# Kernel tuning notes

Measured on AMD Instinct MI355X. Metric: run time of the kernel, lower is better.

The kernel has to match this reference:

```python
import jax, jax.numpy as jnp
import numpy as np
import math

FS, N_FFT, NUM_BANDS, NUM_BINS = 16000, 512, 31, 257
H = 96  # dim_hidden

def band_partition():
    f_min, f_max = FS / N_FFT, FS / 2.0
    z_min = 69.0 + 12.0 * math.log2(f_min / 440.0)
    z_max = 69.0 + 12.0 * math.log2(f_max / 440.0)
    z = np.linspace(z_min, z_max, NUM_BANDS + 2)
    f_points = 440.0 * 2.0 ** ((z - 69.0) / 12.0)
    bins = np.round(f_points * N_FFT / FS).astype(np.int64)
    bins[0] = 0
    bands = []
    for i in range(NUM_BANDS):
        s = max(0, int(bins[i]))
        e = min(NUM_BINS, int(bins[i + 2]) + 1)
        if e <= s:
            e = s + 1
        bands.append((s, e))
    return bands

BANDS = band_partition()

def hann(L):
    # torch.hann_window default (periodic=True)
    return 0.5 - 0.5 * jnp.cos(2.0 * jnp.pi * jnp.arange(L, dtype=jnp.float32) / L)

def chan_ln(x, eps=1e-5):
    # AdaNorm2d assumed = LayerNorm over channel dim, no affine
    m = jnp.mean(x, axis=1, keepdims=True)
    v = jnp.var(x, axis=1, keepdims=True)
    return (x - m) * jax.lax.rsqrt(v + eps)

def prelu(x, a):
    return jnp.where(x >= 0, x, a * x)

def setup_inputs() -> dict:
    key = jax.random.key(0)
    ks = jax.random.split(key, 20)
    B, T = 4, 1000
    return {
        'mix_repr': jax.random.normal(ks[0], (B, H, NUM_BINS, T), jnp.float32),
        'spin': jax.random.normal(ks[1], (B, 64, NUM_BINS, T), jnp.float32),
        'doa': jax.random.normal(ks[2], (B, 36), jnp.float32),
        'enc_w': jax.random.normal(ks[3], (NUM_BANDS, H, 64), jnp.float32) * 0.05,
        'enc_b': jax.random.normal(ks[4], (NUM_BANDS, H), jnp.float32) * 0.05,
        'enc_a': 0.25 * jnp.ones((NUM_BANDS,), jnp.float32),
        'dqg_w': jax.random.normal(ks[5], (NUM_BANDS, 2 * H, 36), jnp.float32) * 0.05,
        'dqg_b': jax.random.normal(ks[6], (NUM_BANDS, 2 * H), jnp.float32) * 0.05,
        'dec_w': jax.random.normal(ks[7], (NUM_BANDS, H, H), jnp.float32) * 0.05,
        'dec_b': jax.random.normal(ks[8], (NUM_BANDS, H), jnp.float32) * 0.05,
        'dec_a': 0.25 * jnp.ones((NUM_BANDS,), jnp.float32),
        'qw': jax.random.normal(ks[9], (H, H), jnp.float32) * 0.05,
        'qb': jax.random.normal(ks[10], (H,), jnp.float32) * 0.05,
        'kw': jax.random.normal(ks[11], (H, H), jnp.float32) * 0.05,
        'kb': jax.random.normal(ks[12], (H,), jnp.float32) * 0.05,
        'vw': jax.random.normal(ks[13], (H, H), jnp.float32) * 0.05,
        'vb': jax.random.normal(ks[14], (H,), jnp.float32) * 0.05,
        'ow': jax.random.normal(ks[15], (H, H), jnp.float32) * 0.05,
        'ob': jax.random.normal(ks[16], (H,), jnp.float32) * 0.05,
    }

def reference(mix_repr, spin, doa, enc_w, enc_b, enc_a, dqg_w, dqg_b,
              dec_w, dec_b, dec_a, qw, qb, kw, kb, vw, vb, ow, ob):
    B, D, F, T = mix_repr.shape
    merged = jnp.zeros((B, H, F, T), mix_repr.dtype)
    wsum = jnp.zeros((F,), mix_repr.dtype)
    for k, (s, e) in enumerate(BANDS):  # fixed set of 31 static ragged bands
        L = e - s
        win = hann(L)
        sub = spin[:, :, s:e, :]                                   # [B,64,L,T]
        feat = jnp.einsum('oc,bcft->boft', enc_w[k], sub) + enc_b[k][None, :, None, None]
        feat = prelu(chan_ln(feat), enc_a[k])
        qp = doa @ dqg_w[k].T + dqg_b[k]                           # [B,2H]
        gamma, beta = qp[:, :H], qp[:, H:]
        tgt = (1.0 + gamma)[:, :, None, None] * feat + beta[:, :, None, None]
        dec = jnp.einsum('oc,bcft->boft', dec_w[k], tgt) + dec_b[k][None, :, None, None]
        dec = prelu(chan_ln(dec), dec_a[k])
        merged = merged.at[:, :, s:e, :].add(dec * win[None, None, :, None])
        wsum = wsum.at[s:e].add(win)
    merged = merged / jnp.clip(wsum, 1e-8)[None, None, :, None]
    # MixtureQueryFusion: 1x1 conv cross-attention gate
    Q = jnp.einsum('oc,bcft->boft', qw, mix_repr) + qb[None, :, None, None]
    K = jnp.einsum('oc,bcft->boft', kw, merged) + kb[None, :, None, None]
    V = jnp.einsum('oc,bcft->boft', vw, merged) + vb[None, :, None, None]
    attn = jax.nn.sigmoid(jnp.sum(Q * K, axis=1, keepdims=True) / jnp.sqrt(jnp.float32(H)))
    attended = V * attn
    out = mix_repr + jnp.einsum('oc,bcft->boft', ow, attended) + ob[None, :, None, None]
    return out
```

## Files before the change

kernel.cpp:

```cpp
#include <hip/hip_runtime.h>
#include <math.h>

#define NBANDS 31
#define FT 257000

typedef __attribute__((ext_vector_type(8))) short bh8;
typedef __attribute__((ext_vector_type(4))) float f4;

__constant__ int d_bs[NBANDS] = {0,1,1,2,2,2,3,3,4,5,6,7,8,10,11,13,16,19,23,27,32,38,45,54,64,76,91,108,128,152,181};
__constant__ int d_be[NBANDS] = {2,3,3,3,4,4,5,6,7,8,9,11,12,14,17,20,24,28,33,39,46,55,65,77,92,109,129,153,182,216,257};

__device__ __forceinline__ unsigned short b16u(float v) {
  __bf16 h = (__bf16)v;
  return __builtin_bit_cast(unsigned short, h);
}
__device__ __forceinline__ unsigned pk2(float a, float b) {
  return (unsigned)b16u(a) | ((unsigned)b16u(b) << 16);
}
__device__ __forceinline__ float hann1(int i, int L) {
  return 0.5f - 0.5f * cosf(6.283185307179586f * (float)i / (float)L);
}

__global__ __launch_bounds__(256) void prep_w(
    const float* __restrict__ enc_w, const float* __restrict__ dec_w,
    const float* __restrict__ qw, const float* __restrict__ kw,
    const float* __restrict__ vw, const float* __restrict__ ow,
    unsigned short* __restrict__ w16) {
  const int stride = gridDim.x * blockDim.x;
  for (int i = blockIdx.x * blockDim.x + threadIdx.x; i < 513024; i += stride) {
    float v;
    if (i < 190464) {
      const int k = i / 6144, r = i - k * 6144;
      const int tile = r >> 9, li = r & 511;
      const int lane = li >> 3, j = li & 7;
      const int g = lane >> 4, n = lane & 15;
      const int mt = tile >> 1, kt = tile & 1;
      v = enc_w[k * 6144 + (mt * 16 + n) * 64 + kt * 32 + g * 8 + j];
    } else if (i < 476160) {
      const int i2 = i - 190464;
      const int k = i2 / 9216, r = i2 - k * 9216;
      const int tile = r >> 9, li = r & 511;
      const int lane = li >> 3, j = li & 7;
      const int g = lane >> 4, n = lane & 15;
      const int mt = tile / 3, kt = tile - mt * 3;
      v = dec_w[k * 9216 + (mt * 16 + n) * 96 + kt * 32 + g * 8 + j];
    } else {
      const int i2 = i - 476160;
      const int a = i2 / 9216, r = i2 - a * 9216;
      const int tile = r >> 9, li = r & 511;
      const int lane = li >> 3, j = li & 7;
      const int g = lane >> 4, n = lane & 15;
      const int mt = tile / 3, kt = tile - mt * 3;
      const float* src = (a == 0) ? qw : (a == 1) ? kw : (a == 2) ? vw : ow;
      v = src[(mt * 16 + n) * 96 + kt * 32 + g * 8 + j];
    }
    w16[i] = b16u(v);
  }
}

__global__ __launch_bounds__(192) void qp_kernel(const float* __restrict__ doa,
                                                 const float* __restrict__ dqg_w,
                                                 const float* __restrict__ dqg_b,
                                                 float* __restrict__ gbuf) {
  const int k = blockIdx.x, b = blockIdx.y;
  const int tid = threadIdx.x;
  __shared__ float sdoa[36];
  if (tid < 36) sdoa[tid] = doa[b * 36 + tid];
  __syncthreads();
  const float* wr = dqg_w + (k * 192 + tid) * 36;
  float acc = dqg_b[k * 192 + tid];
  #pragma unroll
  for (int i = 0; i < 36; ++i) acc = fmaf(wr[i], sdoa[i], acc);
  if (tid < 96) acc += 1.0f;
  gbuf[(k * 4 + b) * 192 + tid] = acc;
}

__global__ __launch_bounds__(320) void tab_kernel(float* __restrict__ ftab) {
  const int f = blockIdx.x * blockDim.x + threadIdx.x;
  if (f >= 257) return;
  int k0 = 0; while (d_be[k0] <= f) ++k0;
  int k1 = k0; while (k1 < NBANDS && d_bs[k1] <= f) ++k1;
  float wsum = 0.f, wn[5];
  for (int k = k0; k < k1; ++k) {
    const float wv = hann1(f - d_bs[k], d_be[k] - d_bs[k]);
    wn[k - k0] = wv; wsum += wv;
  }
  float* o = ftab + f * 8;
  o[0] = (float)k0; o[1] = (float)(k1 - k0); o[2] = 1.0f / fmaxf(wsum, 1e-8f);
  #pragma unroll
  for (int j = 0; j < 5; ++j) o[3 + j] = (j < k1 - k0) ? wn[j] : 0.f;
}

#define LDSWAIT asm volatile("s_waitcnt lgkmcnt(0)" ::: "memory")

__device__ __forceinline__ void init6(f4* acc, const float* s, int off) {
  #pragma unroll
  for (int mt = 0; mt < 6; ++mt) {
    const float4 bb = *reinterpret_cast<const float4*>(s + mt * 16 + off);
    acc[mt] = (f4){bb.x, bb.y, bb.z, bb.w};
  }
}
__device__ __forceinline__ f4 init1(const float* s, int mt, int off) {
  const float4 bb = *reinterpret_cast<const float4*>(s + mt * 16 + off);
  return (f4){bb.x, bb.y, bb.z, bb.w};
}
__device__ __forceinline__ void ln96(const f4* acc, float& mean, float& rs) {
  float sm = 0.f, sq = 0.f;
  #pragma unroll
  for (int mt = 0; mt < 6; ++mt)
    #pragma unroll
    for (int r = 0; r < 4; ++r) { const float v = acc[mt][r]; sm += v; sq = fmaf(v, v, sq); }
  sm += __shfl_xor(sm, 16); sm += __shfl_xor(sm, 32);
  sq += __shfl_xor(sq, 16); sq += __shfl_xor(sq, 32);
  mean = sm * (1.f / 96.f);
  rs = rsqrtf(sq * (1.f / 96.f) - mean * mean + 1e-5f);
}
__device__ __forceinline__ void load6s(bh8* dst, const unsigned short* p, int step9) {
  #pragma unroll
  for (int mt = 0; mt < 6; ++mt)
    dst[mt] = *reinterpret_cast<const bh8*>(p + ((mt * step9) << 9));
}

__global__ __launch_bounds__(256, 4) void fused_mfma(
    const float* __restrict__ mix, const float* __restrict__ spin,
    const unsigned short* __restrict__ enc16, const float* __restrict__ enc_b, const float* __restrict__ enc_a,
    const unsigned short* __restrict__ dec16, const float* __restrict__ dec_b, const float* __restrict__ dec_a,
    const float* __restrict__ gb, const float* __restrict__ ftab,
    const unsigned short* __restrict__ q16, const float* __restrict__ qb,
    const unsigned short* __restrict__ k16, const float* __restrict__ kb,
    const unsigned short* __restrict__ v16, const float* __restrict__ vb,
    const unsigned short* __restrict__ o16, const float* __restrict__ ob,
    float* __restrict__ out) {
  const int id0 = (int)blockIdx.x;
  const int id  = (id0 & 7) * 2056 + (id0 >> 3);
  const int tt  = id & 15;
  const int fb  = id >> 4;
  const int f   = fb % 257;
  const int b   = fb / 257;
  const int t0  = tt << 6;

  const int tid  = threadIdx.x;
  const int lane = tid & 63;
  const int w    = tid >> 6;
  const int g    = lane >> 4;
  const int n    = lane & 15;
  const int col  = (w << 4) + n;
  const int t    = t0 + col;
  const bool tv  = t < 1000;
  const int tcl  = tv ? t : 999;
  const int sw   = (n & 7) << 3;
  const int lb   = lane << 3;

  __shared__ __align__(16) unsigned short XT[64 * 128];
  __shared__ __align__(16) float stage[5 * 512 + 384];
  unsigned short* xw = XT + col * 128;

  const float* ft = ftab + f * 8;
  const int k0 = (int)ft[0];
  const int nb = (int)ft[1];
  const float winv = ft[2];

  {
    const int tot = (nb << 9) + 384;
    for (int i = tid; i < tot; i += 256) {
      const int kk = i >> 9, r = i & 511;
      float v = 0.f;
      if (kk < nb) {
        const int k = k0 + kk;
        if      (r < 96)  v = enc_b[k * 96 + r];
        else if (r < 192) v = dec_b[k * 96 + (r - 96)];
        else if (r < 384) v = gb[(k * 4 + b) * 192 + (r - 192)];
        else if (r == 384) v = enc_a[k];
        else if (r == 385) v = dec_a[k];
        else if (r == 386) v = ft[3 + kk];
      } else {
        const int r2 = i - (nb << 9);
        v = (r2 < 96) ? qb[r2] : (r2 < 192) ? kb[r2 - 96] : (r2 < 288) ? vb[r2 - 192] : ob[r2 - 288];
      }
      stage[i] = v;
    }
  }

  const float* spL = spin + b * 64 * FT + f * 1000 + tcl;
  const float* mxL = mix  + b * 96 * FT + f * 1000 + tcl;

  bh8 spb[2];
  {
    float spf[16];
    #pragma unroll
    for (int j = 0; j < 8; ++j) spf[j]     = __builtin_nontemporal_load(spL + (g * 8 + j) * FT);
    #pragma unroll
    for (int j = 0; j < 8; ++j) spf[8 + j] = __builtin_nontemporal_load(spL + (32 + g * 8 + j) * FT);
    #pragma unroll
    for (int kt = 0; kt < 2; ++kt)
      #pragma unroll
      for (int j = 0; j < 8; ++j) spb[kt][j] = (short)b16u(spf[kt * 8 + j]);
  }

  bh8 pre[6];
  load6s(pre, enc16 + k0 * 6144 + lb, 2);

  __syncthreads();

  f4 macc[6];
  #pragma unroll
  for (int mt = 0; mt < 6; ++mt) macc[mt] = (f4){0.f, 0.f, 0.f, 0.f};

  const int oo = g * 4;

  for (int kk = 0; kk < nb; ++kk) {
    const int k = k0 + kk;
    const unsigned short* ew  = enc16 + k * 6144 + lb;
    const unsigned short* dwp = dec16 + k * 9216 + lb;
    const float* stg = stage + (kk << 9);

    f4 acc[6];
    init6(acc, stg, oo);
    #pragma unroll
    for (int mt = 0; mt < 6; ++mt)
      acc[mt] = __builtin_amdgcn_mfma_f32_16x16x32_bf16(pre[mt], spb[0], acc[mt], 0, 0, 0);
    #pragma unroll
    for (int mt = 0; mt < 6; ++mt) {
      const bh8 af = *reinterpret_cast<const bh8*>(ew + ((mt * 2 + 1) << 9));
      acc[mt] = __builtin_amdgcn_mfma_f32_16x16x32_bf16(af, spb[1], acc[mt], 0, 0, 0);
    }

    load6s(pre, dwp, 3);

    float mean, rs;
    ln96(acc, mean, rs);
    const float ea = stg[384];
    #pragma unroll
    for (int mt = 0; mt < 6; ++mt) {
      const float4 ga = *reinterpret_cast<const float4*>(stg + 192 + mt * 16 + oo);
      const float4 be = *reinterpret_cast<const float4*>(stg + 288 + mt * 16 + oo);
      float x0 = (acc[mt][0] - mean) * rs; x0 = (x0 >= 0.f) ? x0 : ea * x0;
      float x1 = (acc[mt][1] - mean) * rs; x1 = (x1 >= 0.f) ? x1 : ea * x1;
      float x2 = (acc[mt][2] - mean) * rs; x2 = (x2 >= 0.f) ? x2 : ea * x2;
      float x3 = (acc[mt][3] - mean) * rs; x3 = (x3 >= 0.f) ? x3 : ea * x3;
      uint2 u;
      u.x = pk2(fmaf(ga.x, x0, be.x), fmaf(ga.y, x1, be.y));
      u.y = pk2(fmaf(ga.z, x2, be.z), fmaf(ga.w, x3, be.w));
      *reinterpret_cast<uint2*>(xw + ((mt * 16 + g * 4) ^ sw)) = u;
    }
    LDSWAIT;

    f4 dacc[6];
    init6(dacc, stg + 96, oo);
    {
      const bh8 bf0 = *reinterpret_cast<const bh8*>(xw + ((0 * 32 + g * 8) ^ sw));
      #pragma unroll
      for (int mt = 0; mt < 6; ++mt)
        dacc[mt] = __builtin_amdgcn_mfma_f32_16x16x32_bf16(pre[mt], bf0, dacc[mt], 0, 0, 0);
    }

    {
      const bool more = (kk + 1 < nb);
      load6s(pre, more ? (enc16 + (k + 1) * 6144 + lb) : (q16 + lb), more ? 2 : 3);
    }

    #pragma unroll
    for (int kt = 1; kt < 3; ++kt) {
      const bh8 bf = *reinterpret_cast<const bh8*>(xw + ((kt * 32 + g * 8) ^ sw));
      #pragma unroll
      for (int mt = 0; mt < 6; ++mt) {
        const bh8 af = *reinterpret_cast<const bh8*>(dwp + ((mt * 3 + kt) << 9));
        dacc[mt] = __builtin_amdgcn_mfma_f32_16x16x32_bf16(af, bf, dacc[mt], 0, 0, 0);
      }
    }
    float mean2, rs2;
    ln96(dacc, mean2, rs2);
    const float da = stg[385];
    const float win = stg[386];
    #pragma unroll
    for (int mt = 0; mt < 6; ++mt)
      #pragma unroll
      for (int r = 0; r < 4; ++r) {
        float x = (dacc[mt][r] - mean2) * rs2;
        x = (x >= 0.f) ? x : da * x;
        macc[mt][r] = fmaf(win, x, macc[mt][r]);
      }
  }

  bh8 mxb[3];
  {
    float mxf[24];
    #pragma unroll
    for (int kt = 0; kt < 3; ++kt)
      #pragma unroll
      for (int j = 0; j < 8; ++j) mxf[kt * 8 + j] = mxL[(kt * 32 + g * 8 + j) * FT];
    #pragma unroll
    for (int kt = 0; kt < 3; ++kt)
      #pragma unroll
      for (int j = 0; j < 8; ++j) mxb[kt][j] = (short)b16u(mxf[kt * 8 + j]);
  }

  #pragma unroll
  for (int mt = 0; mt < 6; ++mt) {
    uint2 u;
    u.x = pk2(macc[mt][0] * winv, macc[mt][1] * winv);
    u.y = pk2(macc[mt][2] * winv, macc[mt][3] * winv);
    *reinterpret_cast<uint2*>(xw + ((mt * 16 + g * 4) ^ sw)) = u;
  }
  LDSWAIT;
  bh8 gfr[3];
  #pragma unroll
  for (int kt = 0; kt < 3; ++kt) gfr[kt] = *reinterpret_cast<const bh8*>(xw + ((kt * 32 + g * 8) ^ sw));

  const float* stQ = stage + (nb << 9);
  const unsigned short* qp16 = q16 + lb;
  const unsigned short* kp16 = k16 + lb;
  const unsigned short* vp16 = v16 + lb;
  const unsigned short* op16 = o16 + lb;

  float p = 0.f;
  #pragma unroll
  for (int mt = 0; mt < 6; ++mt) {
    f4 qa = init1(stQ, mt, oo);
    qa = __builtin_amdgcn_mfma_f32_16x16x32_bf16(pre[mt], mxb[0], qa, 0, 0, 0);
    #pragma unroll
    for (int kt = 1; kt < 3; ++kt) {
      const bh8 af = *reinterpret_cast<const bh8*>(qp16 + ((mt * 3 + kt) << 9));
      qa = __builtin_amdgcn_mfma_f32_16x16x32_bf16(af, mxb[kt], qa, 0, 0, 0);
    }
    f4 ka = init1(stQ + 96, mt, oo);
    #pragma unroll
    for (int kt = 0; kt < 3; ++kt) {
      const bh8 af = *reinterpret_cast<const bh8*>(kp16 + ((mt * 3 + kt) << 9));
      ka = __builtin_amdgcn_mfma_f32_16x16x32_bf16(af, gfr[kt], ka, 0, 0, 0);
    }
    #pragma unroll
    for (int r = 0; r < 4; ++r) p = fmaf(qa[r], ka[r], p);
  }
  p += __shfl_xor(p, 16); p += __shfl_xor(p, 32);
  const float sig = 1.f / (1.f + __expf(-p * 0.10206207261596575f));

  #pragma unroll
  for (int mt = 0; mt < 6; ++mt) {
    f4 va = init1(stQ + 192, mt, oo);
    #pragma unroll
    for (int kt = 0; kt < 3; ++kt) {
      const bh8 af = *reinterpret_cast<const bh8*>(vp16 + ((mt * 3 + kt) << 9));
      va = __builtin_amdgcn_mfma_f32_16x16x32_bf16(af, gfr[kt], va, 0, 0, 0);
    }
    uint2 u;
    u.x = pk2(va[0] * sig, va[1] * sig);
    u.y = pk2(va[2] * sig, va[3] * sig);
    *reinterpret_cast<uint2*>(xw + ((mt * 16 + g * 4) ^ sw)) = u;
  }
  float mres[6][4];
  #pragma unroll
  for (int mt = 0; mt < 6; ++mt)
    #pragma unroll
    for (int r = 0; r < 4; ++r) mres[mt][r] = mxL[(mt * 16 + g * 4 + r) * FT];
  LDSWAIT;
  bh8 afr[3];
  #pragma unroll
  for (int kt = 0; kt < 3; ++kt) afr[kt] = *reinterpret_cast<const bh8*>(xw + ((kt * 32 + g * 8) ^ sw));

  #pragma unroll
  for (int mt = 0; mt < 6; ++mt) {
    f4 oa = init1(stQ + 288, mt, oo);
    #pragma unroll
    for (int kt = 0; kt < 3; ++kt) {
      const bh8 af = *reinterpret_cast<const bh8*>(op16 + ((mt * 3 + kt) << 9));
      oa = __builtin_amdgcn_mfma_f32_16x16x32_bf16(af, afr[kt], oa, 0, 0, 0);
    }
    if (tv) {
      const int base = (b * 96 + mt * 16 + g * 4) * FT + f * 1000 + t;
      #pragma unroll
      for (int r = 0; r < 4; ++r)
        __builtin_nontemporal_store(mres[mt][r] + oa[r], out + base + r * FT);
    }
  }
}

extern "C" void kernel_launch(void* const* d_in, const int* in_sizes, int n_in,
                              void* d_out, int out_size, void* d_ws, size_t ws_size,
                              hipStream_t stream) {
  (void)in_sizes; (void)n_in; (void)out_size; (void)ws_size;
  const float* mix   = (const float*)d_in[0];
  const float* spin  = (const float*)d_in[1];
  const float* doa   = (const float*)d_in[2];
  const float* enc_w = (const float*)d_in[3];
  const float* enc_b = (const float*)d_in[4];
  const float* enc_a = (const float*)d_in[5];
  const float* dqg_w = (const float*)d_in[6];
  const float* dqg_b = (const float*)d_in[7];
  const float* dec_w = (const float*)d_in[8];
  const float* dec_b = (const float*)d_in[9];
  const float* dec_a = (const float*)d_in[10];
  const float* qw    = (const float*)d_in[11];
  const float* qb    = (const float*)d_in[12];
  const float* kw    = (const float*)d_in[13];
  const float* kb    = (const float*)d_in[14];
  const float* vw    = (const float*)d_in[15];
  const float* vb    = (const float*)d_in[16];
  const float* oww   = (const float*)d_in[17];
  const float* obb   = (const float*)d_in[18];
  float* outp = (float*)d_out;

  unsigned short* w16 = (unsigned short*)d_ws;
  unsigned short* enc16 = w16;
  unsigned short* dec16 = w16 + 190464;
  unsigned short* q16   = w16 + 476160;
  unsigned short* k16   = q16 + 9216;
  unsigned short* v16   = k16 + 9216;
  unsigned short* o16   = v16 + 9216;
  float* gbws = (float*)((char*)d_ws + 1026048);
  float* ftab = (float*)((char*)d_ws + 1121280);

  hipLaunchKernelGGL(prep_w, dim3(512), dim3(256), 0, stream,
                     enc_w, dec_w, qw, kw, vw, oww, w16);
  hipLaunchKernelGGL(qp_kernel, dim3(NBANDS, 4), dim3(192), 0, stream,
                     doa, dqg_w, dqg_b, gbws);
  hipLaunchKernelGGL(tab_kernel, dim3(1), dim3(320), 0, stream, ftab);
  hipLaunchKernelGGL(fused_mfma, dim3(16448), dim3(256), 0, stream,
                     mix, spin, enc16, enc_b, enc_a, dec16, dec_b, dec_a, gbws, ftab,
                     q16, qb, k16, kb, v16, vb, o16, obb, outp);
}
```

Measured before the change: 671.8 us.

## Keep merged accumulator and mix residual in LDS as bf16, drop second mix read

Several changes at once. The band accumulator moves from 24 float registers into a bf16 LDS tile, and the staged biases and gammas are stored as bf16. The mix input, already loaded once for Q, is stashed in LDS and reused as the residual, so the second global read of mix_repr goes away. This cuts global traffic and register pressure, but the residual, the accumulated merge and the biases now carry bf16 rounding error.

```diff
diff --git a/kernel.cpp b/kernel.cpp
--- a/kernel.cpp
+++ b/kernel.cpp
@@ -19,6 +19,15 @@
 }
 __device__ __forceinline__ float hann1(int i, int L) {
   return 0.5f - 0.5f * cosf(6.283185307179586f * (float)i / (float)L);
+}
+__device__ __forceinline__ f4 bf4(const unsigned short* p) {
+  const uint2 u = *reinterpret_cast<const uint2*>(p);
+  f4 r;
+  r[0] = __builtin_bit_cast(float, u.x << 16);
+  r[1] = __builtin_bit_cast(float, u.x & 0xffff0000u);
+  r[2] = __builtin_bit_cast(float, u.y << 16);
+  r[3] = __builtin_bit_cast(float, u.y & 0xffff0000u);
+  return r;
 }
 
 __global__ __launch_bounds__(256) void prep_w(
@@ -93,17 +102,6 @@
 
 #define LDSWAIT asm volatile("s_waitcnt lgkmcnt(0)" ::: "memory")
 
-__device__ __forceinline__ void init6(f4* acc, const float* s, int off) {
-  #pragma unroll
-  for (int mt = 0; mt < 6; ++mt) {
-    const float4 bb = *reinterpret_cast<const float4*>(s + mt * 16 + off);
-    acc[mt] = (f4){bb.x, bb.y, bb.z, bb.w};
-  }
-}
-__device__ __forceinline__ f4 init1(const float* s, int mt, int off) {
-  const float4 bb = *reinterpret_cast<const float4*>(s + mt * 16 + off);
-  return (f4){bb.x, bb.y, bb.z, bb.w};
-}
 __device__ __forceinline__ void ln96(const f4* acc, float& mean, float& rs) {
   float sm = 0.f, sq = 0.f;
   #pragma unroll
@@ -152,8 +150,11 @@
   const int lb   = lane << 3;
 
   __shared__ __align__(16) unsigned short XT[64 * 128];
-  __shared__ __align__(16) float stage[5 * 512 + 384];
+  __shared__ __align__(16) unsigned short MG[64 * 128];
+  __shared__ __align__(16) unsigned short stgb[5 * 512 + 384];
+  __shared__ float sband[5 * 4];
   unsigned short* xw = XT + col * 128;
+  unsigned short* mg = MG + col * 128;
 
   const float* ft = ftab + f * 8;
   const int k0 = (int)ft[0];
@@ -170,14 +171,16 @@
         if      (r < 96)  v = enc_b[k * 96 + r];
         else if (r < 192) v = dec_b[k * 96 + (r - 96)];
         else if (r < 384) v = gb[(k * 4 + b) * 192 + (r - 192)];
-        else if (r == 384) v = enc_a[k];
-        else if (r == 385) v = dec_a[k];
-        else if (r == 386) v = ft[3 + kk];
       } else {
         const int r2 = i - (nb << 9);
         v = (r2 < 96) ? qb[r2] : (r2 < 192) ? kb[r2 - 96] : (r2 < 288) ? vb[r2 - 192] : ob[r2 - 288];
       }
-      stage[i] = v;
+      stgb[i] = b16u(v);
+    }
+    if (tid < nb * 4) {
+      const int kk = tid >> 2, j = tid & 3;
+      sband[tid] = (j == 0) ? enc_a[k0 + kk] : (j == 1) ? dec_a[k0 + kk]
+                 : (j == 2) ? ft[3 + kk] : 0.f;
     }
   }
 
@@ -201,10 +204,6 @@
   load6s(pre, enc16 + k0 * 6144 + lb, 2);
 
   __syncthreads();
-
-  f4 macc[6];
-  #pragma unroll
-  for (int mt = 0; mt < 6; ++mt) macc[mt] = (f4){0.f, 0.f, 0.f, 0.f};
 
   const int oo = g * 4;
 
@@ -212,10 +211,11 @@
     const int k = k0 + kk;
     const unsigned short* ew  = enc16 + k * 6144 + lb;
     const unsigned short* dwp = dec16 + k * 9216 + lb;
-    const float* stg = stage + (kk << 9);
+    const unsigned short* stg = stgb + (kk << 9);
 
     f4 acc[6];
-    init6(acc, stg, oo);
+    #pragma unroll
+    for (int mt = 0; mt < 6; ++mt) acc[mt] = bf4(stg + mt * 16 + oo);
     #pragma unroll
     for (int mt = 0; mt < 6; ++mt)
       acc[mt] = __builtin_amdgcn_mfma_f32_16x16x32_bf16(pre[mt], spb[0], acc[mt], 0, 0, 0);
@@ -229,24 +229,25 @@
 
     float mean, rs;
     ln96(acc, mean, rs);
-    const float ea = stg[384];
+    const float ea = sband[kk * 4];
     #pragma unroll
     for (int mt = 0; mt < 6; ++mt) {
-      const float4 ga = *reinterpret_cast<const float4*>(stg + 192 + mt * 16 + oo);
-      const float4 be = *reinterpret_cast<const float4*>(stg + 288 + mt * 16 + oo);
+      const f4 ga = bf4(stg + 192 + mt * 16 + oo);
+      const f4 be = bf4(stg + 288 + mt * 16 + oo);
       float x0 = (acc[mt][0] - mean) * rs; x0 = (x0 >= 0.f) ? x0 : ea * x0;
       float x1 = (acc[mt][1] - mean) * rs; x1 = (x1 >= 0.f) ? x1 : ea * x1;
       float x2 = (acc[mt][2] - mean) * rs; x2 = (x2 >= 0.f) ? x2 : ea * x2;
       float x3 = (acc[mt][3] - mean) * rs; x3 = (x3 >= 0.f) ? x3 : ea * x3;
       uint2 u;
-      u.x = pk2(fmaf(ga.x, x0, be.x), fmaf(ga.y, x1, be.y));
-      u.y = pk2(fmaf(ga.z, x2, be.z), fmaf(ga.w, x3, be.w));
-      *reinterpret_cast<uint2*>(xw + ((mt * 16 + g * 4) ^ sw)) = u;
+      u.x = pk2(fmaf(ga[0], x0, be[0]), fmaf(ga[1], x1, be[1]));
+      u.y = pk2(fmaf(ga[2], x2, be[2]), fmaf(ga[3], x3, be[3]));
+      *reinterpret_cast<uint2*>(xw + ((mt * 16 + oo) ^ sw)) = u;
     }
     LDSWAIT;
 
     f4 dacc[6];
-    init6(dacc, stg + 96, oo);
+    #pragma unroll
+    for (int mt = 0; mt < 6; ++mt) dacc[mt] = bf4(stg + 96 + mt * 16 + oo);
     {
       const bh8 bf0 = *reinterpret_cast<const bh8*>(xw + ((0 * 32 + g * 8) ^ sw));
       #pragma unroll
@@ -270,16 +271,26 @@
     }
     float mean2, rs2;
     ln96(dacc, mean2, rs2);
-    const float da = stg[385];
-    const float win = stg[386];
-    #pragma unroll
-    for (int mt = 0; mt < 6; ++mt)
-      #pragma unroll
-      for (int r = 0; r < 4; ++r) {
-        float x = (dacc[mt][r] - mean2) * rs2;
-        x = (x >= 0.f) ? x : da * x;
-        macc[mt][r] = fmaf(win, x, macc[mt][r]);
+    const float da  = sband[kk * 4 + 1];
+    const float win = sband[kk * 4 + 2];
+    #pragma unroll
+    for (int mt = 0; mt < 6; ++mt) {
+      float x0 = (dacc[mt][0] - mean2) * rs2; x0 = (x0 >= 0.f) ? x0 : da * x0;
+      float x1 = (dacc[mt][1] - mean2) * rs2; x1 = (x1 >= 0.f) ? x1 : da * x1;
+      float x2 = (dacc[mt][2] - mean2) * rs2; x2 = (x2 >= 0.f) ? x2 : da * x2;
+      float x3 = (dacc[mt][3] - mean2) * rs2; x3 = (x3 >= 0.f) ? x3 : da * x3;
+      unsigned short* mp = mg + ((mt * 16 + oo) ^ sw);
+      uint2 u;
+      if (kk == 0) {
+        u.x = pk2(win * x0, win * x1);
+        u.y = pk2(win * x2, win * x3);
+      } else {
+        const f4 cur = bf4(mp);
+        u.x = pk2(fmaf(win, x0, cur[0]), fmaf(win, x1, cur[1]));
+        u.y = pk2(fmaf(win, x2, cur[2]), fmaf(win, x3, cur[3]));
       }
+      *reinterpret_cast<uint2*>(mp) = u;
+    }
   }
 
   bh8 mxb[3];
@@ -288,7 +299,7 @@
     #pragma unroll
     for (int kt = 0; kt < 3; ++kt)
       #pragma unroll
-      for (int j = 0; j < 8; ++j) mxf[kt * 8 + j] = mxL[(kt * 32 + g * 8 + j) * FT];
+      for (int j = 0; j < 8; ++j) mxf[kt * 8 + j] = __builtin_nontemporal_load(mxL + (kt * 32 + g * 8 + j) * FT);
     #pragma unroll
     for (int kt = 0; kt < 3; ++kt)
       #pragma unroll
@@ -297,17 +308,22 @@
 
   #pragma unroll
   for (int mt = 0; mt < 6; ++mt) {
+    const f4 mv = bf4(mg + ((mt * 16 + oo) ^ sw));
     uint2 u;
-    u.x = pk2(macc[mt][0] * winv, macc[mt][1] * winv);
-    u.y = pk2(macc[mt][2] * winv, macc[mt][3] * winv);
-    *reinterpret_cast<uint2*>(xw + ((mt * 16 + g * 4) ^ sw)) = u;
+    u.x = pk2(mv[0] * winv, mv[1] * winv);
+    u.y = pk2(mv[2] * winv, mv[3] * winv);
+    *reinterpret_cast<uint2*>(xw + ((mt * 16 + oo) ^ sw)) = u;
   }
   LDSWAIT;
   bh8 gfr[3];
   #pragma unroll
   for (int kt = 0; kt < 3; ++kt) gfr[kt] = *reinterpret_cast<const bh8*>(xw + ((kt * 32 + g * 8) ^ sw));
 
-  const float* stQ = stage + (nb << 9);
+  #pragma unroll
+  for (int kt = 0; kt < 3; ++kt)
+    *reinterpret_cast<bh8*>(mg + ((kt * 32 + g * 8) ^ sw)) = mxb[kt];
+
+  const unsigned short* stQ = stgb + (nb << 9);
   const unsigned short* qp16 = q16 + lb;
   const unsigned short* kp16 = k16 + lb;
   const unsigned short* vp16 = v16 + lb;
@@ -316,14 +332,14 @@
   float p = 0.f;
   #pragma unroll
   for (int mt = 0; mt < 6; ++mt) {
-    f4 qa = init1(stQ, mt, oo);
+    f4 qa = bf4(stQ + mt * 16 + oo);
     qa = __builtin_amdgcn_mfma_f32_16x16x32_bf16(pre[mt], mxb[0], qa, 0, 0, 0);
     #pragma unroll
     for (int kt = 1; kt < 3; ++kt) {
       const bh8 af = *reinterpret_cast<const bh8*>(qp16 + ((mt * 3 + kt) << 9));
       qa = __builtin_amdgcn_mfma_f32_16x16x32_bf16(af, mxb[kt], qa, 0, 0, 0);
     }
-    f4 ka = init1(stQ + 96, mt, oo);
+    f4 ka = bf4(stQ + 96 + mt * 16 + oo);
     #pragma unroll
     for (int kt = 0; kt < 3; ++kt) {
       const bh8 af = *reinterpret_cast<const bh8*>(kp16 + ((mt * 3 + kt) << 9));
@@ -337,7 +353,7 @@
 
   #pragma unroll
   for (int mt = 0; mt < 6; ++mt) {
-    f4 va = init1(stQ + 192, mt, oo);
+    f4 va = bf4(stQ + 192 + mt * 16 + oo);
     #pragma unroll
     for (int kt = 0; kt < 3; ++kt) {
       const bh8 af = *reinterpret_cast<const bh8*>(vp16 + ((mt * 3 + kt) << 9));
@@ -346,13 +362,8 @@
     uint2 u;
     u.x = pk2(va[0] * sig, va[1] * sig);
     u.y = pk2(va[2] * sig, va[3] * sig);
-    *reinterpret_cast<uint2*>(xw + ((mt * 16 + g * 4) ^ sw)) = u;
-  }
-  float mres[6][4];
-  #pragma unroll
-  for (int mt = 0; mt < 6; ++mt)
-    #pragma unroll
-    for (int r = 0; r < 4; ++r) mres[mt][r] = mxL[(mt * 16 + g * 4 + r) * FT];
+    *reinterpret_cast<uint2*>(xw + ((mt * 16 + oo) ^ sw)) = u;
+  }
   LDSWAIT;
   bh8 afr[3];
   #pragma unroll
@@ -360,17 +371,18 @@
 
   #pragma unroll
   for (int mt = 0; mt < 6; ++mt) {
-    f4 oa = init1(stQ + 288, mt, oo);
+    f4 oa = bf4(stQ + 288 + mt * 16 + oo);
     #pragma unroll
     for (int kt = 0; kt < 3; ++kt) {
       const bh8 af = *reinterpret_cast<const bh8*>(op16 + ((mt * 3 + kt) << 9));
       oa = __builtin_amdgcn_mfma_f32_16x16x32_bf16(af, afr[kt], oa, 0, 0, 0);
     }
     if (tv) {
-      const int base = (b * 96 + mt * 16 + g * 4) * FT + f * 1000 + t;
+      const f4 mr = bf4(mg + ((mt * 16 + oo) ^ sw));
+      const int base = (b * 96 + mt * 16 + oo) * FT + f * 1000 + t;
       #pragma unroll
       for (int r = 0; r < 4; ++r)
-        __builtin_nontemporal_store(mres[mt][r] + oa[r], out + base + r * FT);
+        __builtin_nontemporal_store(mr[r] + oa[r], out + base + r * FT);
     }
   }
 }
```

Result: faster. 621.3 us (-7.5%).
